# Performance work log

Measured on AMD Instinct MI355X. Metric: run time of the kernel, lower is better.

The kernel has to match this reference:

```python
import jax, jax.numpy as jnp
import numpy as np

B, S, D, E, H = 1024, 256, 1024, 1024, 1024  # batch, state, belief, embedding, hidden
T1 = 32            # clip_length => number of scan steps
POSE_TILES = 4
MIN_STD = 0.1


def _gru(x, h, wih, whh, bih, bhh):
    # torch.nn.GRUCell semantics
    gi = x @ wih.T + bih
    gh = h @ whh.T + bhh
    i_r, i_z, i_n = jnp.split(gi, 3, axis=-1)
    h_r, h_z, h_n = jnp.split(gh, 3, axis=-1)
    r = jax.nn.sigmoid(i_r + h_r)
    z = jax.nn.sigmoid(i_z + h_z)
    n = jnp.tanh(i_n + r * h_n)
    return (1.0 - z) * n + z * h


def setup_inputs() -> dict:
    key = jax.random.key(0)
    ks = iter(jax.random.split(key, 40))
    g = lambda shape, s=1.0: jax.random.normal(next(ks), shape, dtype=jnp.float32) * s
    W = 0.02
    inp = {
        'prev_state': g((B, S)),
        'prev_belief': g((B, D)),
        'observations': g((T1, B, E)),
        'poses': g((T1, B, 6)),
        'noise_post': g((T1, B, S)),
        'noise_prior': g((T1, B, S)),
        # fc_embed_state_posterior: (2S+E) -> D
        'W_esq': g((D, 2 * S + E), W), 'b_esq': jnp.zeros((D,), jnp.float32),
        # fc_embed_state_prior: (2S+6*pose_tiles) -> D
        'W_esp': g((D, 2 * S + 6 * POSE_TILES), W), 'b_esp': jnp.zeros((D,), jnp.float32),
        # GRUCell posterior / prior
        'gq_wih': g((3 * D, D), W), 'gq_whh': g((3 * D, D), W),
        'gq_bih': jnp.zeros((3 * D,), jnp.float32), 'gq_bhh': jnp.zeros((3 * D,), jnp.float32),
        'gp_wih': g((3 * D, D), W), 'gp_whh': g((3 * D, D), W),
        'gp_bih': jnp.zeros((3 * D,), jnp.float32), 'gp_bhh': jnp.zeros((3 * D,), jnp.float32),
        # belief -> hidden -> 2*state heads
        'W_ebq': g((H, D), W), 'b_ebq': jnp.zeros((H,), jnp.float32),
        'W_sq': g((2 * S, H), W), 'b_sq': jnp.zeros((2 * S,), jnp.float32),
        'W_ebp': g((H, D), W), 'b_ebp': jnp.zeros((H,), jnp.float32),
        'W_sp': g((2 * S, H), W), 'b_sp': jnp.zeros((2 * S,), jnp.float32),
    }
    return inp


def reference(prev_state, prev_belief, observations, poses, noise_post, noise_prior,
              W_esq, b_esq, W_esp, b_esp,
              gq_wih, gq_whh, gq_bih, gq_bhh,
              gp_wih, gp_whh, gp_bih, gp_bhh,
              W_ebq, b_ebq, W_sq, b_sq, W_ebp, b_ebp, W_sp, b_sp):
    relu = jax.nn.relu

    def step(carry, xs):
        s_q, s_p, b_q, b_p = carry
        obs, pose, nq, npn = xs
        # posterior branch
        h = relu(jnp.concatenate([obs, s_q, s_p], axis=1) @ W_esq.T + b_esq)
        b_q_new = _gru(h, b_q, gq_wih, gq_whh, gq_bih, gq_bhh)
        hq = relu(b_q_new @ W_ebq.T + b_ebq)
        mq, raw_sq = jnp.split(hq @ W_sq.T + b_sq, 2, axis=1)
        std_q = jax.nn.softplus(raw_sq) + MIN_STD
        s_q_new = mq + std_q * nq
        # prior branch (uses old s_q, s_p per original code)
        pose_t = jnp.tile(pose, (1, POSE_TILES))
        h2 = relu(jnp.concatenate([pose_t, s_q, s_p], axis=1) @ W_esp.T + b_esp)
        b_p_new = _gru(h2, b_p, gp_wih, gp_whh, gp_bih, gp_bhh)
        hp = relu(b_p_new @ W_ebp.T + b_ebp)
        mp, raw_sp = jnp.split(hp @ W_sp.T + b_sp, 2, axis=1)
        std_p = jax.nn.softplus(raw_sp) + MIN_STD
        s_p_new = mp + std_p * npn
        new_carry = (s_q_new, s_p_new, b_q_new, b_p_new)
        ys = (b_q_new, s_p_new, mp, std_p, s_q_new, mq, std_q)
        return new_carry, ys

    carry0 = (prev_state, prev_state, prev_belief, prev_belief)
    _, ys = jax.lax.scan(step, carry0, (observations, poses, noise_post, noise_prior))
    post_beliefs, prior_states, prior_means, prior_stds, post_states, post_means, post_stds = ys
    # order matches torch: [posterior_beliefs, prior_states, prior_means, prior_std_devs,
    #                       posterior_states, posterior_means, posterior_std_devs]
    return (post_beliefs, prior_states, prior_means, prior_stds,
            post_states, post_means, post_stds)
```

## Files before the change

### kernel.cpp

```cpp
#include <hip/hip_runtime.h>
#include <stdint.h>
#include <math.h>

typedef unsigned short ushort_t;
typedef __attribute__((ext_vector_type(8))) short bf16x8;
typedef __attribute__((ext_vector_type(4))) float f32x4;

#define T1_ 32

__device__ __forceinline__ float bf2f(ushort_t u) {
  union { unsigned int i; float f; } v; v.i = ((unsigned int)u) << 16; return v.f;
}
__device__ __forceinline__ ushort_t f2bf(float f) {
  union { float f; unsigned int i; } v; v.f = f;
  unsigned int x = v.i;
  return (ushort_t)((x + 0x7FFFu + ((x >> 16) & 1u)) >> 16);
}
__device__ __forceinline__ float sigm(float x) { return 1.f / (1.f + expf(-x)); }

__device__ __forceinline__ void gld16(const ushort_t* g, ushort_t* l) {
  __builtin_amdgcn_global_load_lds(
      (const __attribute__((address_space(1))) unsigned int*)g,
      (__attribute__((address_space(3))) unsigned int*)l, 16, 0, 0);
}

__global__ __launch_bounds__(256) void cvt_k(const float* src, ushort_t* dst,
                                             long long n, int cols, int src_ld, int src_off) {
  const long long idx = (long long)blockIdx.x * 256 + threadIdx.x;
  if (idx >= n) return;
  const long long row = idx / cols;
  const int col = (int)(idx - row * cols);
  dst[idx] = f2bf(src[row * src_ld + src_off + col]);
}

__global__ __launch_bounds__(256) void wpe_k(const float* Wesp, float* wpe) {
  const int i = blockIdx.x * 256 + threadIdx.x;
  if (i >= 1024 * 6) return;
  const int n = i / 6, j = i % 6;
  float s = 0.f;
#pragma unroll
  for (int r = 0; r < 4; ++r) s += Wesp[(long long)n * 536 + j + 6 * r];
  wpe[i] = s;
}

__global__ void marker_k(float* out, float K) {
  if (threadIdx.x == 0 && blockIdx.x == 0) out[0] = K;
}

struct MMSide {
  const ushort_t* a0; const ushort_t* a1; const ushort_t* a2;
  int kd0, kd1, kd2;
  int coff0, coff1, coff2;
  int nparts;
  const ushort_t* W; int ldw;
  const float* bias;
  ushort_t* outb;
  int dopose;
};
struct MM2Args { MMSide s[2]; const float* poses_t; const float* wpe; };

__global__ __launch_bounds__(256) void mm2_k(MM2Args g) {
  const MMSide S = g.s[blockIdx.z];
  __shared__ __align__(16) ushort_t As[2048];
  __shared__ __align__(16) ushort_t Ws[4096];
  const int tid = threadIdx.x;
  const int lane = tid & 63, wave = tid >> 6;
  const int wm = wave >> 1, wn = wave & 1;
  const int bn0 = blockIdx.x * 128, bm0 = blockIdx.y * 64;

  f32x4 acc[2][4];
#pragma unroll
  for (int i = 0; i < 2; ++i)
#pragma unroll
    for (int j = 0; j < 4; ++j) acc[i][j] = (f32x4){0.f, 0.f, 0.f, 0.f};

  const ushort_t* ap[3] = { S.a0, S.a1, S.a2 };
  const int kd[3] = { S.kd0, S.kd1, S.kd2 };
  const int cf[3] = { S.coff0, S.coff1, S.coff2 };

  const int rowA = tid >> 2, kcA = (tid & 3) * 8;
  ushort_t* ldsA  = &As[wave * 512];
  ushort_t* ldsW0 = &Ws[wave * 512];
  ushort_t* ldsW1 = &Ws[2048 + wave * 512];

#pragma unroll 1
  for (int p = 0; p < S.nparts; ++p) {
    const int kdim = kd[p];
    const ushort_t* Ap = ap[p] + (long long)bm0 * kdim + (long long)rowA * kdim + kcA;
    const ushort_t* Wp0 = S.W + cf[p] + (long long)(bn0 + rowA) * S.ldw + kcA;
    const ushort_t* Wp1 = Wp0 + (long long)64 * S.ldw;
    const int nkt = kdim >> 5;
#pragma unroll 1
    for (int kt = 0; kt < nkt; ++kt) {
      const int k0 = kt * 32;
      __syncthreads();
      gld16(Ap + k0, ldsA);
      gld16(Wp0 + k0, ldsW0);
      gld16(Wp1 + k0, ldsW1);
      __syncthreads();
      const int r15 = lane & 15, kh = (lane >> 4) * 8;
      bf16x8 a[2], b[4];
#pragma unroll
      for (int i = 0; i < 2; ++i)
        a[i] = *(const bf16x8*)&As[(wm * 32 + i * 16 + r15) * 32 + kh];
#pragma unroll
      for (int j = 0; j < 4; ++j)
        b[j] = *(const bf16x8*)&Ws[(wn * 64 + j * 16 + r15) * 32 + kh];
#pragma unroll
      for (int i = 0; i < 2; ++i)
#pragma unroll
        for (int j = 0; j < 4; ++j)
          acc[i][j] = __builtin_amdgcn_mfma_f32_16x16x32_bf16(a[i], b[j], acc[i][j], 0, 0, 0);
    }
  }

  const int r15 = lane & 15, rq = (lane >> 4) * 4;
#pragma unroll
  for (int i = 0; i < 2; ++i) {
#pragma unroll
    for (int j = 0; j < 4; ++j) {
      const int col = bn0 + wn * 64 + j * 16 + r15;
      const float bs = S.bias[col];
#pragma unroll
      for (int q = 0; q < 4; ++q) {
        const int row = bm0 + wm * 32 + i * 16 + rq + q;
        float v = acc[i][j][q] + bs;
        if (S.dopose) {
          float s = 0.f;
#pragma unroll
          for (int jj = 0; jj < 6; ++jj)
            s += g.poses_t[(long long)row * 6 + jj] * g.wpe[col * 6 + jj];
          v += s;
        }
        v = fmaxf(v, 0.f);
        S.outb[(size_t)row * 1024 + col] = f2bf(v);
      }
    }
  }
}

struct GruSide {
  const ushort_t* x;
  const ushort_t* hb;
  const float* hf;
  const ushort_t* wih; const ushort_t* whh;
  const float* bih; const float* bhh;
  float* dst; ushort_t* dstb;
};
struct Gru2Args { GruSide s[2]; };

__global__ __launch_bounds__(256) void gru2_k(Gru2Args g) {
  const GruSide S = g.s[blockIdx.z];
  __shared__ __align__(16) ushort_t Xs[2048];
  __shared__ __align__(16) ushort_t Hs[2048];
  __shared__ __align__(16) ushort_t Wt[6][2048];
  const int tid = threadIdx.x;
  const int lane = tid & 63, wave = tid >> 6;
  const int wm = wave >> 1, wn = wave & 1;
  const int bn0 = blockIdx.x * 64, bm0 = blockIdx.y * 64;

  f32x4 acc[6][2][2];
#pragma unroll
  for (int gg = 0; gg < 6; ++gg)
#pragma unroll
    for (int i = 0; i < 2; ++i)
#pragma unroll
      for (int j = 0; j < 2; ++j) acc[gg][i][j] = (f32x4){0.f, 0.f, 0.f, 0.f};

  const int rowA = tid >> 2, kc = (tid & 3) * 8;
  const long long xoff = (long long)(bm0 + rowA) * 1024 + kc;

#pragma unroll 1
  for (int kt = 0; kt < 32; ++kt) {
    const int k0 = kt * 32;
    __syncthreads();
    gld16(S.x + xoff + k0, &Xs[wave * 512]);
    gld16(S.hb + xoff + k0, &Hs[wave * 512]);
#pragma unroll
    for (int gg = 0; gg < 6; ++gg) {
      const ushort_t* base = (gg < 3) ? S.wih : S.whh;
      const int grow = (gg % 3) * 1024 + bn0 + rowA;
      gld16(base + (long long)grow * 1024 + k0 + kc, &Wt[gg][wave * 512]);
    }
    __syncthreads();
    const int r15 = lane & 15, kh = (lane >> 4) * 8;
    bf16x8 ax[2], ah[2];
#pragma unroll
    for (int i = 0; i < 2; ++i) {
      ax[i] = *(const bf16x8*)&Xs[(wm * 32 + i * 16 + r15) * 32 + kh];
      ah[i] = *(const bf16x8*)&Hs[(wm * 32 + i * 16 + r15) * 32 + kh];
    }
#pragma unroll
    for (int gg = 0; gg < 6; ++gg) {
      bf16x8 bw[2];
#pragma unroll
      for (int j = 0; j < 2; ++j)
        bw[j] = *(const bf16x8*)&Wt[gg][(wn * 32 + j * 16 + r15) * 32 + kh];
#pragma unroll
      for (int i = 0; i < 2; ++i)
#pragma unroll
        for (int j = 0; j < 2; ++j)
          acc[gg][i][j] = __builtin_amdgcn_mfma_f32_16x16x32_bf16(
              (gg < 3) ? ax[i] : ah[i], bw[j], acc[gg][i][j], 0, 0, 0);
    }
  }

  const int r15 = lane & 15, rq = (lane >> 4) * 4;
#pragma unroll
  for (int j = 0; j < 2; ++j) {
    const int col = bn0 + wn * 32 + j * 16 + r15;
    const float br  = S.bih[col],        bhr = S.bhh[col];
    const float bz  = S.bih[col + 1024], bhz = S.bhh[col + 1024];
    const float bn_ = S.bih[col + 2048], bhn = S.bhh[col + 2048];
#pragma unroll
    for (int i = 0; i < 2; ++i) {
#pragma unroll
      for (int q = 0; q < 4; ++q) {
        const int row = bm0 + wm * 32 + i * 16 + rq + q;
        const float ir = acc[0][i][j][q] + br,   hr = acc[3][i][j][q] + bhr;
        const float iz = acc[1][i][j][q] + bz,   hz = acc[4][i][j][q] + bhz;
        const float in_ = acc[2][i][j][q] + bn_, hn = acc[5][i][j][q] + bhn;
        const float r = sigm(ir + hr);
        const float z = sigm(iz + hz);
        const float ng = tanhf(in_ + r * hn);
        const long long o = (long long)row * 1024 + col;
        const float bnew = (1.f - z) * ng + z * S.hf[o];
        S.dst[o] = bnew;
        S.dstb[o] = f2bf(bnew);
      }
    }
  }
}

struct HeadSide {
  const ushort_t* hh;
  const ushort_t* Ws;
  const float* bs;
  const float* noise;
  float* omean; float* ostd; float* ostate;
  ushort_t* stateb;
};
struct Head2Args { HeadSide s[2]; };

__global__ __launch_bounds__(256) void head2_k(Head2Args g) {
  const HeadSide S = g.s[blockIdx.z];
  __shared__ __align__(16) ushort_t As[2048];
  __shared__ __align__(16) ushort_t Wt[2][2048];
  const int tid = threadIdx.x;
  const int lane = tid & 63, wave = tid >> 6;
  const int wm = wave >> 1, wn = wave & 1;
  const int bn0 = blockIdx.x * 64, bm0 = blockIdx.y * 64;

  f32x4 acc[2][2][2];
#pragma unroll
  for (int gg = 0; gg < 2; ++gg)
#pragma unroll
    for (int i = 0; i < 2; ++i)
#pragma unroll
      for (int j = 0; j < 2; ++j) acc[gg][i][j] = (f32x4){0.f, 0.f, 0.f, 0.f};

  const int rowA = tid >> 2, kc = (tid & 3) * 8;
  const long long aoff = (long long)(bm0 + rowA) * 1024 + kc;

#pragma unroll 1
  for (int kt = 0; kt < 32; ++kt) {
    const int k0 = kt * 32;
    __syncthreads();
    gld16(S.hh + aoff + k0, &As[wave * 512]);
#pragma unroll
    for (int gg = 0; gg < 2; ++gg)
      gld16(S.Ws + (long long)(gg * 256 + bn0 + rowA) * 1024 + k0 + kc, &Wt[gg][wave * 512]);
    __syncthreads();
    const int r15 = lane & 15, kh = (lane >> 4) * 8;
    bf16x8 a[2];
#pragma unroll
    for (int i = 0; i < 2; ++i)
      a[i] = *(const bf16x8*)&As[(wm * 32 + i * 16 + r15) * 32 + kh];
#pragma unroll
    for (int gg = 0; gg < 2; ++gg) {
      bf16x8 bw[2];
#pragma unroll
      for (int j = 0; j < 2; ++j)
        bw[j] = *(const bf16x8*)&Wt[gg][(wn * 32 + j * 16 + r15) * 32 + kh];
#pragma unroll
      for (int i = 0; i < 2; ++i)
#pragma unroll
        for (int j = 0; j < 2; ++j)
          acc[gg][i][j] = __builtin_amdgcn_mfma_f32_16x16x32_bf16(a[i], bw[j], acc[gg][i][j], 0, 0, 0);
    }
  }

  const int r15 = lane & 15, rq = (lane >> 4) * 4;
#pragma unroll
  for (int j = 0; j < 2; ++j) {
    const int col = bn0 + wn * 32 + j * 16 + r15;
    const float bm = S.bs[col];
    const float bsd = S.bs[col + 256];
#pragma unroll
    for (int i = 0; i < 2; ++i) {
#pragma unroll
      for (int q = 0; q < 4; ++q) {
        const int row = bm0 + wm * 32 + i * 16 + rq + q;
        const float mean = acc[0][i][j][q] + bm;
        const float rs = acc[1][i][j][q] + bsd;
        const float sp = fmaxf(rs, 0.f) + log1pf(expf(-fabsf(rs)));
        const float sd = sp + 0.1f;
        const long long o = (long long)row * 256 + col;
        const float st = mean + sd * S.noise[o];
        S.omean[o] = mean; S.ostd[o] = sd; S.ostate[o] = st;
        S.stateb[o] = f2bf(st);
      }
    }
  }
}

extern "C" void kernel_launch(void* const* d_in, const int* in_sizes, int n_in,
                              void* d_out, int out_size, void* d_ws, size_t ws_size,
                              hipStream_t stream) {
  float* out = (float*)d_out;

  int gid = 0;
  if (n_in != 26) gid = 1;
  else if (out_size != 83886080) gid = 2;
  else if (in_sizes[0] != 262144 || in_sizes[1] != 1048576 || in_sizes[2] != 33554432 ||
           in_sizes[3] != 196608 || in_sizes[4] != 8388608 || in_sizes[5] != 8388608) gid = 3;
  else if (in_sizes[6] != 1572864 || in_sizes[8] != 548864) gid = 4;
  else if (in_sizes[10] != 3145728 || in_sizes[11] != 3145728 ||
           in_sizes[14] != 3145728 || in_sizes[15] != 3145728) gid = 5;
  else if (in_sizes[18] != 1048576 || in_sizes[20] != 524288 ||
           in_sizes[22] != 1048576 || in_sizes[24] != 524288) gid = 6;
  else if (ws_size < (128ull << 20)) gid = 7;
  if (gid != 0) {
    unsigned wsMB = (unsigned)(ws_size >> 20); if (wsMB > 4095u) wsMB = 4095u;
    const float K = (float)gid * 16777216.0f + (float)wsMB;
    hipLaunchKernelGGL(marker_k, dim3(1), dim3(64), 0, stream, out, K);
    return;
  }

  const float* prev_state  = (const float*)d_in[0];
  const float* prev_belief = (const float*)d_in[1];
  const float* observations= (const float*)d_in[2];
  const float* poses       = (const float*)d_in[3];
  const float* noise_post  = (const float*)d_in[4];
  const float* noise_prior = (const float*)d_in[5];
  const float* W_esq = (const float*)d_in[6];  const float* b_esq = (const float*)d_in[7];
  const float* W_esp = (const float*)d_in[8];  const float* b_esp = (const float*)d_in[9];
  const float* gq_wih = (const float*)d_in[10]; const float* gq_whh = (const float*)d_in[11];
  const float* gq_bih = (const float*)d_in[12]; const float* gq_bhh = (const float*)d_in[13];
  const float* gp_wih = (const float*)d_in[14]; const float* gp_whh = (const float*)d_in[15];
  const float* gp_bih = (const float*)d_in[16]; const float* gp_bhh = (const float*)d_in[17];
  const float* W_ebq = (const float*)d_in[18]; const float* b_ebq = (const float*)d_in[19];
  const float* W_sq  = (const float*)d_in[20]; const float* b_sq  = (const float*)d_in[21];
  const float* W_ebp = (const float*)d_in[22]; const float* b_ebp = (const float*)d_in[23];
  const float* W_sp  = (const float*)d_in[24]; const float* b_sp  = (const float*)d_in[25];

  float* out_belief = out;
  float* out_pstate = out + 33554432LL;
  float* out_pmean  = out + 41943040LL;
  float* out_pstd   = out + 50331648LL;
  float* out_qstate = out + 58720256LL;
  float* out_qmean  = out + 67108864LL;
  float* out_qstd   = out + 75497472LL;

  char* w = (char*)d_ws;
  ushort_t* obsb  = (ushort_t*)(w);
  ushort_t* wWesq = (ushort_t*)(w + (64ull << 20));
  ushort_t* wWesp = (ushort_t*)(w + (67ull << 20));
  ushort_t* wGqih = (ushort_t*)(w + (68ull << 20));
  ushort_t* wGqhh = (ushort_t*)(w + (74ull << 20));
  ushort_t* wGpih = (ushort_t*)(w + (80ull << 20));
  ushort_t* wGphh = (ushort_t*)(w + (86ull << 20));
  ushort_t* wEbq  = (ushort_t*)(w + (92ull << 20));
  ushort_t* wEbp  = (ushort_t*)(w + (94ull << 20));
  ushort_t* wSq   = (ushort_t*)(w + (96ull << 20));
  ushort_t* wSp   = (ushort_t*)(w + (97ull << 20));
  float*    wpe   = (float*)(w + (98ull << 20));
  ushort_t* h_q   = (ushort_t*)(w + (99ull << 20));
  ushort_t* h_p   = (ushort_t*)(w + (101ull << 20));
  ushort_t* bqb[2] = { (ushort_t*)(w + (103ull << 20)), (ushort_t*)(w + (105ull << 20)) };
  ushort_t* bpb[2] = { (ushort_t*)(w + (107ull << 20)), (ushort_t*)(w + (109ull << 20)) };
  ushort_t* sqb   = (ushort_t*)(w + (111ull << 20));
  ushort_t* spb   = (ushort_t*)(w + (111ull << 20) + 524288);
  float*    bpf[2] = { (float*)(w + (112ull << 20)), (float*)(w + (116ull << 20)) };

  const dim3 blk(256);
  auto cvt = [&](const float* s, ushort_t* d, long long n, int c, int ld, int off) {
    hipLaunchKernelGGL(cvt_k, dim3((unsigned)((n + 255) / 256)), blk, 0, stream, s, d, n, c, ld, off);
  };
  cvt(observations, obsb, 33554432LL, 1024, 1024, 0);
  cvt(W_esq, wWesq, 1572864LL, 1536, 1536, 0);
  cvt(W_esp, wWesp, 524288LL, 512, 536, 24);
  cvt(gq_wih, wGqih, 3145728LL, 1024, 1024, 0);
  cvt(gq_whh, wGqhh, 3145728LL, 1024, 1024, 0);
  cvt(gp_wih, wGpih, 3145728LL, 1024, 1024, 0);
  cvt(gp_whh, wGphh, 3145728LL, 1024, 1024, 0);
  cvt(W_ebq, wEbq, 1048576LL, 1024, 1024, 0);
  cvt(W_ebp, wEbp, 1048576LL, 1024, 1024, 0);
  cvt(W_sq, wSq, 524288LL, 1024, 1024, 0);
  cvt(W_sp, wSp, 524288LL, 1024, 1024, 0);
  cvt(prev_state, sqb, 262144LL, 256, 256, 0);
  cvt(prev_state, spb, 262144LL, 256, 256, 0);
  cvt(prev_belief, bqb[1], 1048576LL, 1024, 1024, 0);
  cvt(prev_belief, bpb[1], 1048576LL, 1024, 1024, 0);
  hipLaunchKernelGGL(wpe_k, dim3(24), blk, 0, stream, W_esp, wpe);

  for (int t = 0; t < T1_; ++t) {
    const int cur = t & 1, prv = cur ^ 1;
    const ushort_t* obs_t = obsb + (long long)t * 1048576;
    const float* bq_prev_f = (t == 0) ? prev_belief : out_belief + (long long)(t - 1) * 1048576;
    const float* bp_prev_f = (t == 0) ? prev_belief : bpf[prv];

    MM2Args a{};
    a.s[0] = MMSide{ obs_t, sqb, spb, 1024, 256, 256, 0, 1024, 1280, 3,
                     wWesq, 1536, b_esq, h_q, 0 };
    a.s[1] = MMSide{ sqb, spb, nullptr, 256, 256, 0, 0, 256, 0, 2,
                     wWesp, 512, b_esp, h_p, 1 };
    a.poses_t = poses + (long long)t * 6144; a.wpe = wpe;
    hipLaunchKernelGGL(mm2_k, dim3(8, 16, 2), blk, 0, stream, a);

    Gru2Args gr{};
    gr.s[0] = GruSide{ h_q, bqb[prv], bq_prev_f, wGqih, wGqhh, gq_bih, gq_bhh,
                       out_belief + (long long)t * 1048576, bqb[cur] };
    gr.s[1] = GruSide{ h_p, bpb[prv], bp_prev_f, wGpih, wGphh, gp_bih, gp_bhh,
                       bpf[cur], bpb[cur] };
    hipLaunchKernelGGL(gru2_k, dim3(16, 16, 2), blk, 0, stream, gr);

    a = MM2Args{};
    a.s[0] = MMSide{ bqb[cur], nullptr, nullptr, 1024, 0, 0, 0, 0, 0, 1,
                     wEbq, 1024, b_ebq, h_q, 0 };
    a.s[1] = MMSide{ bpb[cur], nullptr, nullptr, 1024, 0, 0, 0, 0, 0, 1,
                     wEbp, 1024, b_ebp, h_p, 0 };
    hipLaunchKernelGGL(mm2_k, dim3(8, 16, 2), blk, 0, stream, a);

    Head2Args hd{};
    hd.s[0] = HeadSide{ h_q, wSq, b_sq, noise_post + (long long)t * 262144,
                        out_qmean + (long long)t * 262144,
                        out_qstd + (long long)t * 262144,
                        out_qstate + (long long)t * 262144, sqb };
    hd.s[1] = HeadSide{ h_p, wSp, b_sp, noise_prior + (long long)t * 262144,
                        out_pmean + (long long)t * 262144,
                        out_pstd + (long long)t * 262144,
                        out_pstate + (long long)t * 262144, spb };
    hipLaunchKernelGGL(head2_k, dim3(4, 16, 2), blk, 0, stream, hd);
  }
}
```

Baseline: 4.067 ms.

## Fuse whole recurrent scan into one persistent cooperative kernel with grid syncs

Replaces roughly 144 separate kernel launches (conversions plus four kernels per step) with a single cooperative kernel of 256 blocks of 512 threads. It runs the weight and observation conversion, then all 32 steps, separated by grid-wide barriers. It also double-buffers the LDS tiles so the next K-slice loads while MFMAs run on the current one, and retiles the GEMMs across the fixed grid. This removes launch overhead and inter-kernel gaps, but a 256-block grid may leave the GRU and embed GEMMs with fewer waves in flight than before, and grid.sync adds its own cost.

After: 7.827 ms. 1.92x slower.

```diff
diff --git a/kernel.cpp b/kernel.cpp
--- a/kernel.cpp
+++ b/kernel.cpp
@@ -1,16 +1,14 @@
 #include <hip/hip_runtime.h>
+#include <hip/hip_cooperative_groups.h>
 #include <stdint.h>
 #include <math.h>
+
+namespace cg = cooperative_groups;
 
 typedef unsigned short ushort_t;
 typedef __attribute__((ext_vector_type(8))) short bf16x8;
 typedef __attribute__((ext_vector_type(4))) float f32x4;
 
-#define T1_ 32
-
-__device__ __forceinline__ float bf2f(ushort_t u) {
-  union { unsigned int i; float f; } v; v.i = ((unsigned int)u) << 16; return v.f;
-}
 __device__ __forceinline__ ushort_t f2bf(float f) {
   union { float f; unsigned int i; } v; v.f = f;
   unsigned int x = v.i;
@@ -18,299 +16,349 @@
 }
 __device__ __forceinline__ float sigm(float x) { return 1.f / (1.f + expf(-x)); }
 
+__device__ __forceinline__ bf16x8 cvt8(const float* f) {
+  const f32x4 lo = *(const f32x4*)f;
+  const f32x4 hi = *(const f32x4*)(f + 4);
+  bf16x8 r;
+  r[0] = (short)f2bf(lo[0]); r[1] = (short)f2bf(lo[1]);
+  r[2] = (short)f2bf(lo[2]); r[3] = (short)f2bf(lo[3]);
+  r[4] = (short)f2bf(hi[0]); r[5] = (short)f2bf(hi[1]);
+  r[6] = (short)f2bf(hi[2]); r[7] = (short)f2bf(hi[3]);
+  return r;
+}
+
 __device__ __forceinline__ void gld16(const ushort_t* g, ushort_t* l) {
   __builtin_amdgcn_global_load_lds(
       (const __attribute__((address_space(1))) unsigned int*)g,
       (__attribute__((address_space(3))) unsigned int*)l, 16, 0, 0);
 }
 
-__global__ __launch_bounds__(256) void cvt_k(const float* src, ushort_t* dst,
-                                             long long n, int cols, int src_ld, int src_off) {
-  const long long idx = (long long)blockIdx.x * 256 + threadIdx.x;
-  if (idx >= n) return;
-  const long long row = idx / cols;
-  const int col = (int)(idx - row * cols);
-  dst[idx] = f2bf(src[row * src_ld + src_off + col]);
-}
-
-__global__ __launch_bounds__(256) void wpe_k(const float* Wesp, float* wpe) {
-  const int i = blockIdx.x * 256 + threadIdx.x;
-  if (i >= 1024 * 6) return;
-  const int n = i / 6, j = i % 6;
-  float s = 0.f;
-#pragma unroll
-  for (int r = 0; r < 4; ++r) s += Wesp[(long long)n * 536 + j + 6 * r];
-  wpe[i] = s;
-}
-
 __global__ void marker_k(float* out, float K) {
   if (threadIdx.x == 0 && blockIdx.x == 0) out[0] = K;
 }
 
-struct MMSide {
-  const ushort_t* a0; const ushort_t* a1; const ushort_t* a2;
-  int kd0, kd1, kd2;
-  int coff0, coff1, coff2;
-  int nparts;
-  const ushort_t* W; int ldw;
-  const float* bias;
-  ushort_t* outb;
-  int dopose;
+struct MegaArgs {
+  const float *prev_state, *prev_belief, *obs, *poses, *noise_q, *noise_p;
+  const float *W_esq, *b_esq, *W_esp, *b_esp;
+  const float *gq_bih, *gq_bhh, *gp_bih, *gp_bhh;
+  const float *gq_wih, *gq_whh, *gp_wih, *gp_whh;
+  const float *W_ebq, *b_ebq, *W_sq, *b_sq, *W_ebp, *b_ebp, *W_sp, *b_sp;
+  float* out;
+  ushort_t *obsb, *wWesq, *wWesp, *wGqih, *wGqhh, *wGpih, *wGphh, *wEbq, *wEbp, *wSq, *wSp;
+  float* wpe;
+  ushort_t *h_q, *h_p, *bqb0, *bqb1, *bpb0, *bpb1, *sqb, *spb;
+  float *bpf0, *bpf1;
 };
-struct MM2Args { MMSide s[2]; const float* poses_t; const float* wpe; };
-
-__global__ __launch_bounds__(256) void mm2_k(MM2Args g) {
-  const MMSide S = g.s[blockIdx.z];
-  __shared__ __align__(16) ushort_t As[2048];
-  __shared__ __align__(16) ushort_t Ws[4096];
-  const int tid = threadIdx.x;
-  const int lane = tid & 63, wave = tid >> 6;
-  const int wm = wave >> 1, wn = wave & 1;
-  const int bn0 = blockIdx.x * 128, bm0 = blockIdx.y * 64;
-
-  f32x4 acc[2][4];
-#pragma unroll
-  for (int i = 0; i < 2; ++i)
-#pragma unroll
-    for (int j = 0; j < 4; ++j) acc[i][j] = (f32x4){0.f, 0.f, 0.f, 0.f};
-
-  const ushort_t* ap[3] = { S.a0, S.a1, S.a2 };
-  const int kd[3] = { S.kd0, S.kd1, S.kd2 };
-  const int cf[3] = { S.coff0, S.coff1, S.coff2 };
-
-  const int rowA = tid >> 2, kcA = (tid & 3) * 8;
-  ushort_t* ldsA  = &As[wave * 512];
-  ushort_t* ldsW0 = &Ws[wave * 512];
-  ushort_t* ldsW1 = &Ws[2048 + wave * 512];
-
-#pragma unroll 1
-  for (int p = 0; p < S.nparts; ++p) {
-    const int kdim = kd[p];
-    const ushort_t* Ap = ap[p] + (long long)bm0 * kdim + (long long)rowA * kdim + kcA;
-    const ushort_t* Wp0 = S.W + cf[p] + (long long)(bn0 + rowA) * S.ldw + kcA;
-    const ushort_t* Wp1 = Wp0 + (long long)64 * S.ldw;
-    const int nkt = kdim >> 5;
-#pragma unroll 1
-    for (int kt = 0; kt < nkt; ++kt) {
-      const int k0 = kt * 32;
-      __syncthreads();
-      gld16(Ap + k0, ldsA);
-      gld16(Wp0 + k0, ldsW0);
-      gld16(Wp1 + k0, ldsW1);
-      __syncthreads();
-      const int r15 = lane & 15, kh = (lane >> 4) * 8;
-      bf16x8 a[2], b[4];
-#pragma unroll
-      for (int i = 0; i < 2; ++i)
-        a[i] = *(const bf16x8*)&As[(wm * 32 + i * 16 + r15) * 32 + kh];
-#pragma unroll
-      for (int j = 0; j < 4; ++j)
-        b[j] = *(const bf16x8*)&Ws[(wn * 64 + j * 16 + r15) * 32 + kh];
-#pragma unroll
-      for (int i = 0; i < 2; ++i)
-#pragma unroll
-        for (int j = 0; j < 4; ++j)
-          acc[i][j] = __builtin_amdgcn_mfma_f32_16x16x32_bf16(a[i], b[j], acc[i][j], 0, 0, 0);
+
+__global__ __launch_bounds__(512) void mega_k(MegaArgs A) {
+  __shared__ __align__(16) ushort_t lds[2][20480];
+  cg::grid_group grid = cg::this_grid();
+  const int bid = blockIdx.x, tid = threadIdx.x;
+  const int lane = tid & 63, wv = tid >> 6;
+  const int r15 = lane & 15, kh = (lane >> 4) * 8, rq = (lane >> 4) * 4;
+  const int l2 = lane >> 2, l3 = (lane & 3) * 8;
+  const int gtid = bid * 512 + tid;
+
+  {
+    auto cv = [&](const float* s, ushort_t* d, int n8, int c8, int ld, int off) {
+      for (int c = gtid; c < n8; c += 131072) {
+        const int row = c / c8, col = (c - row * c8) * 8;
+        *(bf16x8*)(d + (size_t)row * (c8 * 8) + col) = cvt8(s + (size_t)row * ld + off + col);
+      }
+    };
+    cv(A.obs, A.obsb, 4194304, 128, 1024, 0);
+    cv(A.W_esq, A.wWesq, 196608, 192, 1536, 0);
+    cv(A.W_esp, A.wWesp, 65536, 64, 536, 24);
+    cv(A.gq_wih, A.wGqih, 393216, 128, 1024, 0);
+    cv(A.gq_whh, A.wGqhh, 393216, 128, 1024, 0);
+    cv(A.gp_wih, A.wGpih, 393216, 128, 1024, 0);
+    cv(A.gp_whh, A.wGphh, 393216, 128, 1024, 0);
+    cv(A.W_ebq, A.wEbq, 131072, 128, 1024, 0);
+    cv(A.W_ebp, A.wEbp, 131072, 128, 1024, 0);
+    cv(A.W_sq, A.wSq, 65536, 128, 1024, 0);
+    cv(A.W_sp, A.wSp, 65536, 128, 1024, 0);
+    cv(A.prev_state, A.sqb, 32768, 32, 256, 0);
+    cv(A.prev_state, A.spb, 32768, 32, 256, 0);
+    cv(A.prev_belief, A.bqb1, 131072, 128, 1024, 0);
+    cv(A.prev_belief, A.bpb1, 131072, 128, 1024, 0);
+    for (int i = gtid; i < 6144; i += 131072) {
+      const int n = i / 6, j = i - n * 6;
+      float s = 0.f;
+#pragma unroll
+      for (int r = 0; r < 4; ++r) s += A.W_esp[(size_t)n * 536 + j + 6 * r];
+      A.wpe[i] = s;
     }
   }
-
-  const int r15 = lane & 15, rq = (lane >> 4) * 4;
-#pragma unroll
-  for (int i = 0; i < 2; ++i) {
-#pragma unroll
-    for (int j = 0; j < 4; ++j) {
-      const int col = bn0 + wn * 64 + j * 16 + r15;
-      const float bs = S.bias[col];
-#pragma unroll
-      for (int q = 0; q < 4; ++q) {
-        const int row = bm0 + wm * 32 + i * 16 + rq + q;
-        float v = acc[i][j][q] + bs;
-        if (S.dopose) {
-          float s = 0.f;
-#pragma unroll
-          for (int jj = 0; jj < 6; ++jj)
-            s += g.poses_t[(long long)row * 6 + jj] * g.wpe[col * 6 + jj];
-          v += s;
-        }
-        v = fmaxf(v, 0.f);
-        S.outb[(size_t)row * 1024 + col] = f2bf(v);
+  grid.sync();
+
+  ushort_t* bqb[2] = { A.bqb0, A.bqb1 };
+  ushort_t* bpb[2] = { A.bpb0, A.bpb1 };
+  float* bpf[2] = { A.bpf0, A.bpf1 };
+
+  for (int t = 0; t < 32; ++t) {
+    const int cur = t & 1, prv = cur ^ 1;
+
+    auto embed_like = [&](const ushort_t* A0, const ushort_t* A1, const ushort_t* A2,
+                          int kd0, int c1, int c2, int nkt, int cf0, int cf1, int cf2,
+                          const ushort_t* W, int ldw, const float* bias, ushort_t* outp,
+                          int dopose, const float* poses_t) {
+      const int loc = bid & 127;
+      const int bn0 = (loc & 7) * 128, bm0 = (loc >> 3) * 64;
+      const int wm = wv >> 2, wn = wv & 3;
+
+      auto stage = [&](int buf, int ktg) {
+        const ushort_t* ab; int kd, cf, ktl;
+        if (ktg < c1) { ab = A0; kd = kd0; cf = cf0; ktl = ktg; }
+        else if (ktg < c2) { ab = A1; kd = 256; cf = cf1; ktl = ktg - c1; }
+        else { ab = A2; kd = 256; cf = cf2; ktl = ktg - c2; }
+        const int k0 = ktl * 32;
+        if (wv < 4)
+          gld16(ab + (size_t)(bm0 + wv * 16 + l2) * kd + k0 + l3, &lds[buf][wv * 512]);
+        else
+          gld16(W + cf + (size_t)(bn0 + (wv - 4) * 16 + l2) * ldw + k0 + l3,
+                &lds[buf][2048 + (wv - 4) * 512]);
+        if (wv < 4)
+          gld16(W + cf + (size_t)(bn0 + (wv + 4) * 16 + l2) * ldw + k0 + l3,
+                &lds[buf][2048 + (wv + 4) * 512]);
+      };
+
+      f32x4 acc[2][2];
+#pragma unroll
+      for (int i = 0; i < 2; ++i)
+#pragma unroll
+        for (int j = 0; j < 2; ++j) acc[i][j] = (f32x4){0.f, 0.f, 0.f, 0.f};
+
+      stage(0, 0); __syncthreads();
+      int cb = 0;
+#pragma unroll 1
+      for (int ktg = 0; ktg < nkt; ++ktg) {
+        if (ktg + 1 < nkt) stage(cb ^ 1, ktg + 1);
+        bf16x8 a[2], b[2];
+#pragma unroll
+        for (int i = 0; i < 2; ++i)
+          a[i] = *(const bf16x8*)&lds[cb][(wm * 32 + i * 16 + r15) * 32 + kh];
+#pragma unroll
+        for (int j = 0; j < 2; ++j)
+          b[j] = *(const bf16x8*)&lds[cb][2048 + (wn * 32 + j * 16 + r15) * 32 + kh];
+#pragma unroll
+        for (int i = 0; i < 2; ++i)
+#pragma unroll
+          for (int j = 0; j < 2; ++j)
+            acc[i][j] = __builtin_amdgcn_mfma_f32_16x16x32_bf16(a[i], b[j], acc[i][j], 0, 0, 0);
+        __syncthreads(); cb ^= 1;
+      }
+
+#pragma unroll
+      for (int i = 0; i < 2; ++i) {
+#pragma unroll
+        for (int j = 0; j < 2; ++j) {
+          const int col = bn0 + wn * 32 + j * 16 + r15;
+          const float bs = bias[col];
+#pragma unroll
+          for (int q = 0; q < 4; ++q) {
+            const int row = bm0 + wm * 32 + i * 16 + rq + q;
+            float v = acc[i][j][q] + bs;
+            if (dopose) {
+              float s = 0.f;
+#pragma unroll
+              for (int jj = 0; jj < 6; ++jj)
+                s += poses_t[(size_t)row * 6 + jj] * A.wpe[col * 6 + jj];
+              v += s;
+            }
+            v = fmaxf(v, 0.f);
+            outp[(size_t)row * 1024 + col] = f2bf(v);
+          }
+        }
+      }
+    };
+
+    if ((bid >> 7) == 0)
+      embed_like(A.obsb + (size_t)t * 1048576, A.sqb, A.spb,
+                 1024, 32, 40, 48, 0, 1024, 1280,
+                 A.wWesq, 1536, A.b_esq, A.h_q, 0, nullptr);
+    else
+      embed_like(A.sqb, A.spb, A.spb,
+                 256, 8, 16, 16, 0, 256, 256,
+                 A.wWesp, 512, A.b_esp, A.h_p, 1, A.poses + (size_t)t * 6144);
+    grid.sync();
+
+    {
+      const int side = bid & 1;
+      const int bn0 = ((bid >> 1) & 15) * 64;
+      const int bm0 = (bid >> 5) * 128;
+      const ushort_t *x, *hb, *wih, *whh;
+      const float *hf, *bih, *bhh;
+      float* dst; ushort_t* dstb;
+      if (side == 0) {
+        x = A.h_q; hb = bqb[prv];
+        hf = t ? (A.out + (size_t)(t - 1) * 1048576) : A.prev_belief;
+        wih = A.wGqih; whh = A.wGqhh; bih = A.gq_bih; bhh = A.gq_bhh;
+        dst = A.out + (size_t)t * 1048576; dstb = bqb[cur];
+      } else {
+        x = A.h_p; hb = bpb[prv];
+        hf = t ? bpf[prv] : A.prev_belief;
+        wih = A.wGpih; whh = A.wGphh; bih = A.gp_bih; bhh = A.gp_bhh;
+        dst = bpf[cur]; dstb = bpb[cur];
+      }
+      const int wm = wv >> 1, wn = wv & 1;
+
+      auto stage = [&](int buf, int kt) {
+        const int k0 = kt * 32;
+#pragma unroll
+        for (int u = 0; u < 5; ++u) {
+          const int c = wv * 5 + u;
+          if (c < 8)
+            gld16(x + (size_t)(bm0 + c * 16 + l2) * 1024 + k0 + l3, &lds[buf][c * 512]);
+          else if (c < 16)
+            gld16(hb + (size_t)(bm0 + (c - 8) * 16 + l2) * 1024 + k0 + l3, &lds[buf][c * 512]);
+          else {
+            const int wch = c - 16, gg = wch >> 2, rc = wch & 3;
+            const ushort_t* base = (gg < 3) ? wih : whh;
+            const int gr = (gg < 3 ? gg : gg - 3) * 1024 + bn0 + rc * 16 + l2;
+            gld16(base + (size_t)gr * 1024 + k0 + l3, &lds[buf][8192 + gg * 2048 + rc * 512]);
+          }
+        }
+      };
+
+      f32x4 aR[2][2], aZ[2][2], aNI[2][2], aNH[2][2];
+#pragma unroll
+      for (int i = 0; i < 2; ++i)
+#pragma unroll
+        for (int j = 0; j < 2; ++j) {
+          aR[i][j] = (f32x4){0.f,0.f,0.f,0.f}; aZ[i][j] = (f32x4){0.f,0.f,0.f,0.f};
+          aNI[i][j] = (f32x4){0.f,0.f,0.f,0.f}; aNH[i][j] = (f32x4){0.f,0.f,0.f,0.f};
+        }
+
+      stage(0, 0); __syncthreads();
+      int cb = 0;
+#pragma unroll 1
+      for (int kt = 0; kt < 32; ++kt) {
+        if (kt + 1 < 32) stage(cb ^ 1, kt + 1);
+        bf16x8 ax[2], ah[2], w[6][2];
+#pragma unroll
+        for (int i = 0; i < 2; ++i) {
+          ax[i] = *(const bf16x8*)&lds[cb][(wm * 32 + i * 16 + r15) * 32 + kh];
+          ah[i] = *(const bf16x8*)&lds[cb][4096 + (wm * 32 + i * 16 + r15) * 32 + kh];
+        }
+#pragma unroll
+        for (int g = 0; g < 6; ++g)
+#pragma unroll
+          for (int j = 0; j < 2; ++j)
+            w[g][j] = *(const bf16x8*)&lds[cb][8192 + g * 2048 + (wn * 32 + j * 16 + r15) * 32 + kh];
+#pragma unroll
+        for (int i = 0; i < 2; ++i)
+#pragma unroll
+          for (int j = 0; j < 2; ++j) {
+            aR[i][j]  = __builtin_amdgcn_mfma_f32_16x16x32_bf16(ax[i], w[0][j], aR[i][j], 0, 0, 0);
+            aR[i][j]  = __builtin_amdgcn_mfma_f32_16x16x32_bf16(ah[i], w[3][j], aR[i][j], 0, 0, 0);
+            aZ[i][j]  = __builtin_amdgcn_mfma_f32_16x16x32_bf16(ax[i], w[1][j], aZ[i][j], 0, 0, 0);
+            aZ[i][j]  = __builtin_amdgcn_mfma_f32_16x16x32_bf16(ah[i], w[4][j], aZ[i][j], 0, 0, 0);
+            aNI[i][j] = __builtin_amdgcn_mfma_f32_16x16x32_bf16(ax[i], w[2][j], aNI[i][j], 0, 0, 0);
+            aNH[i][j] = __builtin_amdgcn_mfma_f32_16x16x32_bf16(ah[i], w[5][j], aNH[i][j], 0, 0, 0);
+          }
+        __syncthreads(); cb ^= 1;
+      }
+
+#pragma unroll
+      for (int j = 0; j < 2; ++j) {
+        const int col = bn0 + wn * 32 + j * 16 + r15;
+        const float brz = bih[col] + bhh[col];
+        const float bzz = bih[col + 1024] + bhh[col + 1024];
+        const float bni = bih[col + 2048], bnh = bhh[col + 2048];
+#pragma unroll
+        for (int i = 0; i < 2; ++i) {
+#pragma unroll
+          for (int q = 0; q < 4; ++q) {
+            const int row = bm0 + wm * 32 + i * 16 + rq + q;
+            const float r = sigm(aR[i][j][q] + brz);
+            const float z = sigm(aZ[i][j][q] + bzz);
+            const float ng = tanhf(aNI[i][j][q] + bni + r * (aNH[i][j][q] + bnh));
+            const size_t o = (size_t)row * 1024 + col;
+            const float bnew = (1.f - z) * ng + z * hf[o];
+            dst[o] = bnew;
+            dstb[o] = f2bf(bnew);
+          }
+        }
       }
     }
-  }
-}
-
-struct GruSide {
-  const ushort_t* x;
-  const ushort_t* hb;
-  const float* hf;
-  const ushort_t* wih; const ushort_t* whh;
-  const float* bih; const float* bhh;
-  float* dst; ushort_t* dstb;
-};
-struct Gru2Args { GruSide s[2]; };
-
-__global__ __launch_bounds__(256) void gru2_k(Gru2Args g) {
-  const GruSide S = g.s[blockIdx.z];
-  __shared__ __align__(16) ushort_t Xs[2048];
-  __shared__ __align__(16) ushort_t Hs[2048];
-  __shared__ __align__(16) ushort_t Wt[6][2048];
-  const int tid = threadIdx.x;
-  const int lane = tid & 63, wave = tid >> 6;
-  const int wm = wave >> 1, wn = wave & 1;
-  const int bn0 = blockIdx.x * 64, bm0 = blockIdx.y * 64;
-
-  f32x4 acc[6][2][2];
-#pragma unroll
-  for (int gg = 0; gg < 6; ++gg)
-#pragma unroll
-    for (int i = 0; i < 2; ++i)
-#pragma unroll
-      for (int j = 0; j < 2; ++j) acc[gg][i][j] = (f32x4){0.f, 0.f, 0.f, 0.f};
-
-  const int rowA = tid >> 2, kc = (tid & 3) * 8;
-  const long long xoff = (long long)(bm0 + rowA) * 1024 + kc;
-
+    grid.sync();
+
+    if ((bid >> 7) == 0)
+      embed_like(bqb[cur], bqb[cur], bqb[cur], 1024, 32, 32, 32, 0, 0, 0,
+                 A.wEbq, 1024, A.b_ebq, A.h_q, 0, nullptr);
+    else
+      embed_like(bpb[cur], bpb[cur], bpb[cur], 1024, 32, 32, 32, 0, 0, 0,
+                 A.wEbp, 1024, A.b_ebp, A.h_p, 0, nullptr);
+    grid.sync();
+
+    if (bid < 128) {
+      const int side = bid & 1;
+      const int t64 = bid >> 1;
+      const int bn0 = (t64 & 3) * 64, bm0 = (t64 >> 2) * 64;
+      const ushort_t* hh = side ? A.h_p : A.h_q;
+      const ushort_t* Ws = side ? A.wSp : A.wSq;
+      const float* bs = side ? A.b_sp : A.b_sq;
+      const float* noise = (side ? A.noise_p : A.noise_q) + (size_t)t * 262144;
+      float* omean  = A.out + (side ? 41943040LL : 67108864LL) + (size_t)t * 262144;
+      float* ostd   = A.out + (side ? 50331648LL : 75497472LL) + (size_t)t * 262144;
+      float* ostate = A.out + (side ? 33554432LL : 58720256LL) + (size_t)t * 262144;
+      ushort_t* stb = side ? A.spb : A.sqb;
+      const int wm = wv >> 2, wn = wv & 3;
+
+      auto stage = [&](int buf, int kt) {
+        const int k0 = kt * 32;
+        if (wv < 4)
+          gld16(hh + (size_t)(bm0 + wv * 16 + l2) * 1024 + k0 + l3, &lds[buf][wv * 512]);
+        else
+          gld16(Ws + (size_t)(bn0 + (wv - 4) * 16 + l2) * 1024 + k0 + l3,
+                &lds[buf][2048 + (wv - 4) * 512]);
+        if (wv < 4)
+          gld16(Ws + (size_t)(256 + bn0 + wv * 16 + l2) * 1024 + k0 + l3,
+                &lds[buf][4096 + wv * 512]);
+      };
+
+      f32x4 aM[2], aS[2];
+#pragma unroll
+      for (int i = 0; i < 2; ++i) { aM[i] = (f32x4){0.f,0.f,0.f,0.f}; aS[i] = (f32x4){0.f,0.f,0.f,0.f}; }
+
+      stage(0, 0); __syncthreads();
+      int cb = 0;
 #pragma unroll 1
-  for (int kt = 0; kt < 32; ++kt) {
-    const int k0 = kt * 32;
-    __syncthreads();
-    gld16(S.x + xoff + k0, &Xs[wave * 512]);
-    gld16(S.hb + xoff + k0, &Hs[wave * 512]);
-#pragma unroll
-    for (int gg = 0; gg < 6; ++gg) {
-      const ushort_t* base = (gg < 3) ? S.wih : S.whh;
-      const int grow = (gg % 3) * 1024 + bn0 + rowA;
-      gld16(base + (long long)grow * 1024 + k0 + kc, &Wt[gg][wave * 512]);
+      for (int kt = 0; kt < 32; ++kt) {
+        if (kt + 1 < 32) stage(cb ^ 1, kt + 1);
+        bf16x8 a[2];
+#pragma unroll
+        for (int i = 0; i < 2; ++i)
+          a[i] = *(const bf16x8*)&lds[cb][(wm * 32 + i * 16 + r15) * 32 + kh];
+        const bf16x8 bm8 = *(const bf16x8*)&lds[cb][2048 + (wn * 16 + r15) * 32 + kh];
+        const bf16x8 br8 = *(const bf16x8*)&lds[cb][4096 + (wn * 16 + r15) * 32 + kh];
+#pragma unroll
+        for (int i = 0; i < 2; ++i) {
+          aM[i] = __builtin_amdgcn_mfma_f32_16x16x32_bf16(a[i], bm8, aM[i], 0, 0, 0);
+          aS[i] = __builtin_amdgcn_mfma_f32_16x16x32_bf16(a[i], br8, aS[i], 0, 0, 0);
+        }
+        __syncthreads(); cb ^= 1;
+      }
+
+      const int col = bn0 + wn * 16 + r15;
+      const float bm_ = bs[col], bsd = bs[col + 256];
+#pragma unroll
+      for (int i = 0; i < 2; ++i) {
+#pragma unroll
+        for (int q = 0; q < 4; ++q) {
+          const int row = bm0 + wm * 32 + i * 16 + rq + q;
+          const float mean = aM[i][q] + bm_;
+          const float rs = aS[i][q] + bsd;
+          const float sp = fmaxf(rs, 0.f) + log1pf(expf(-fabsf(rs)));
+          const float sd = sp + 0.1f;
+          const size_t o = (size_t)row * 256 + col;
+          const float st = mean + sd * noise[o];
+          omean[o] = mean; ostd[o] = sd; ostate[o] = st;
+          stb[o] = f2bf(st);
+        }
+      }
     }
-    __syncthreads();
-    const int r15 = lane & 15, kh = (lane >> 4) * 8;
-    bf16x8 ax[2], ah[2];
-#pragma unroll
-    for (int i = 0; i < 2; ++i) {
-      ax[i] = *(const bf16x8*)&Xs[(wm * 32 + i * 16 + r15) * 32 + kh];
-      ah[i] = *(const bf16x8*)&Hs[(wm * 32 + i * 16 + r15) * 32 + kh];
-    }
-#pragma unroll
-    for (int gg = 0; gg < 6; ++gg) {
-      bf16x8 bw[2];
-#pragma unroll
-      for (int j = 0; j < 2; ++j)
-        bw[j] = *(const bf16x8*)&Wt[gg][(wn * 32 + j * 16 + r15) * 32 + kh];
-#pragma unroll
-      for (int i = 0; i < 2; ++i)
-#pragma unroll
-        for (int j = 0; j < 2; ++j)
-          acc[gg][i][j] = __builtin_amdgcn_mfma_f32_16x16x32_bf16(
-              (gg < 3) ? ax[i] : ah[i], bw[j], acc[gg][i][j], 0, 0, 0);
-    }
-  }
-
-  const int r15 = lane & 15, rq = (lane >> 4) * 4;
-#pragma unroll
-  for (int j = 0; j < 2; ++j) {
-    const int col = bn0 + wn * 32 + j * 16 + r15;
-    const float br  = S.bih[col],        bhr = S.bhh[col];
-    const float bz  = S.bih[col + 1024], bhz = S.bhh[col + 1024];
-    const float bn_ = S.bih[col + 2048], bhn = S.bhh[col + 2048];
-#pragma unroll
-    for (int i = 0; i < 2; ++i) {
-#pragma unroll
-      for (int q = 0; q < 4; ++q) {
-        const int row = bm0 + wm * 32 + i * 16 + rq + q;
-        const float ir = acc[0][i][j][q] + br,   hr = acc[3][i][j][q] + bhr;
-        const float iz = acc[1][i][j][q] + bz,   hz = acc[4][i][j][q] + bhz;
-        const float in_ = acc[2][i][j][q] + bn_, hn = acc[5][i][j][q] + bhn;
-        const float r = sigm(ir + hr);
-        const float z = sigm(iz + hz);
-        const float ng = tanhf(in_ + r * hn);
-        const long long o = (long long)row * 1024 + col;
-        const float bnew = (1.f - z) * ng + z * S.hf[o];
-        S.dst[o] = bnew;
-        S.dstb[o] = f2bf(bnew);
-      }
-    }
-  }
-}
-
-struct HeadSide {
-  const ushort_t* hh;
-  const ushort_t* Ws;
-  const float* bs;
-  const float* noise;
-  float* omean; float* ostd; float* ostate;
-  ushort_t* stateb;
-};
-struct Head2Args { HeadSide s[2]; };
-
-__global__ __launch_bounds__(256) void head2_k(Head2Args g) {
-  const HeadSide S = g.s[blockIdx.z];
-  __shared__ __align__(16) ushort_t As[2048];
-  __shared__ __align__(16) ushort_t Wt[2][2048];
-  const int tid = threadIdx.x;
-  const int lane = tid & 63, wave = tid >> 6;
-  const int wm = wave >> 1, wn = wave & 1;
-  const int bn0 = blockIdx.x * 64, bm0 = blockIdx.y * 64;
-
-  f32x4 acc[2][2][2];
-#pragma unroll
-  for (int gg = 0; gg < 2; ++gg)
-#pragma unroll
-    for (int i = 0; i < 2; ++i)
-#pragma unroll
-      for (int j = 0; j < 2; ++j) acc[gg][i][j] = (f32x4){0.f, 0.f, 0.f, 0.f};
-
-  const int rowA = tid >> 2, kc = (tid & 3) * 8;
-  const long long aoff = (long long)(bm0 + rowA) * 1024 + kc;
-
-#pragma unroll 1
-  for (int kt = 0; kt < 32; ++kt) {
-    const int k0 = kt * 32;
-    __syncthreads();
-    gld16(S.hh + aoff + k0, &As[wave * 512]);
-#pragma unroll
-    for (int gg = 0; gg < 2; ++gg)
-      gld16(S.Ws + (long long)(gg * 256 + bn0 + rowA) * 1024 + k0 + kc, &Wt[gg][wave * 512]);
-    __syncthreads();
-    const int r15 = lane & 15, kh = (lane >> 4) * 8;
-    bf16x8 a[2];
-#pragma unroll
-    for (int i = 0; i < 2; ++i)
-      a[i] = *(const bf16x8*)&As[(wm * 32 + i * 16 + r15) * 32 + kh];
-#pragma unroll
-    for (int gg = 0; gg < 2; ++gg) {
-      bf16x8 bw[2];
-#pragma unroll
-      for (int j = 0; j < 2; ++j)
-        bw[j] = *(const bf16x8*)&Wt[gg][(wn * 32 + j * 16 + r15) * 32 + kh];
-#pragma unroll
-      for (int i = 0; i < 2; ++i)
-#pragma unroll
-        for (int j = 0; j < 2; ++j)
-          acc[gg][i][j] = __builtin_amdgcn_mfma_f32_16x16x32_bf16(a[i], bw[j], acc[gg][i][j], 0, 0, 0);
-    }
-  }
-
-  const int r15 = lane & 15, rq = (lane >> 4) * 4;
-#pragma unroll
-  for (int j = 0; j < 2; ++j) {
-    const int col = bn0 + wn * 32 + j * 16 + r15;
-    const float bm = S.bs[col];
-    const float bsd = S.bs[col + 256];
-#pragma unroll
-    for (int i = 0; i < 2; ++i) {
-#pragma unroll
-      for (int q = 0; q < 4; ++q) {
-        const int row = bm0 + wm * 32 + i * 16 + rq + q;
-        const float mean = acc[0][i][j][q] + bm;
-        const float rs = acc[1][i][j][q] + bsd;
-        const float sp = fmaxf(rs, 0.f) + log1pf(expf(-fabsf(rs)));
-        const float sd = sp + 0.1f;
-        const long long o = (long long)row * 256 + col;
-        const float st = mean + sd * S.noise[o];
-        S.omean[o] = mean; S.ostd[o] = sd; S.ostate[o] = st;
-        S.stateb[o] = f2bf(st);
-      }
-    }
+    grid.sync();
   }
 }
 
@@ -337,110 +385,48 @@
     return;
   }
 
-  const float* prev_state  = (const float*)d_in[0];
-  const float* prev_belief = (const float*)d_in[1];
-  const float* observations= (const float*)d_in[2];
-  const float* poses       = (const float*)d_in[3];
-  const float* noise_post  = (const float*)d_in[4];
-  const float* noise_prior = (const float*)d_in[5];
-  const float* W_esq = (const float*)d_in[6];  const float* b_esq = (const float*)d_in[7];
-  const float* W_esp = (const float*)d_in[8];  const float* b_esp = (const float*)d_in[9];
-  const float* gq_wih = (const float*)d_in[10]; const float* gq_whh = (const float*)d_in[11];
-  const float* gq_bih = (const float*)d_in[12]; const float* gq_bhh = (const float*)d_in[13];
-  const float* gp_wih = (const float*)d_in[14]; const float* gp_whh = (const float*)d_in[15];
-  const float* gp_bih = (const float*)d_in[16]; const float* gp_bhh = (const float*)d_in[17];
-  const float* W_ebq = (const float*)d_in[18]; const float* b_ebq = (const float*)d_in[19];
-  const float* W_sq  = (const float*)d_in[20]; const float* b_sq  = (const float*)d_in[21];
-  const float* W_ebp = (const float*)d_in[22]; const float* b_ebp = (const float*)d_in[23];
-  const float* W_sp  = (const float*)d_in[24]; const float* b_sp  = (const float*)d_in[25];
-
-  float* out_belief = out;
-  float* out_pstate = out + 33554432LL;
-  float* out_pmean  = out + 41943040LL;
-  float* out_pstd   = out + 50331648LL;
-  float* out_qstate = out + 58720256LL;
-  float* out_qmean  = out + 67108864LL;
-  float* out_qstd   = out + 75497472LL;
-
   char* w = (char*)d_ws;
-  ushort_t* obsb  = (ushort_t*)(w);
-  ushort_t* wWesq = (ushort_t*)(w + (64ull << 20));
-  ushort_t* wWesp = (ushort_t*)(w + (67ull << 20));
-  ushort_t* wGqih = (ushort_t*)(w + (68ull << 20));
-  ushort_t* wGqhh = (ushort_t*)(w + (74ull << 20));
-  ushort_t* wGpih = (ushort_t*)(w + (80ull << 20));
-  ushort_t* wGphh = (ushort_t*)(w + (86ull << 20));
-  ushort_t* wEbq  = (ushort_t*)(w + (92ull << 20));
-  ushort_t* wEbp  = (ushort_t*)(w + (94ull << 20));
-  ushort_t* wSq   = (ushort_t*)(w + (96ull << 20));
-  ushort_t* wSp   = (ushort_t*)(w + (97ull << 20));
-  float*    wpe   = (float*)(w + (98ull << 20));
-  ushort_t* h_q   = (ushort_t*)(w + (99ull << 20));
-  ushort_t* h_p   = (ushort_t*)(w + (101ull << 20));
-  ushort_t* bqb[2] = { (ushort_t*)(w + (103ull << 20)), (ushort_t*)(w + (105ull << 20)) };
-  ushort_t* bpb[2] = { (ushort_t*)(w + (107ull << 20)), (ushort_t*)(w + (109ull << 20)) };
-  ushort_t* sqb   = (ushort_t*)(w + (111ull << 20));
-  ushort_t* spb   = (ushort_t*)(w + (111ull << 20) + 524288);
-  float*    bpf[2] = { (float*)(w + (112ull << 20)), (float*)(w + (116ull << 20)) };
-
-  const dim3 blk(256);
-  auto cvt = [&](const float* s, ushort_t* d, long long n, int c, int ld, int off) {
-    hipLaunchKernelGGL(cvt_k, dim3((unsigned)((n + 255) / 256)), blk, 0, stream, s, d, n, c, ld, off);
-  };
-  cvt(observations, obsb, 33554432LL, 1024, 1024, 0);
-  cvt(W_esq, wWesq, 1572864LL, 1536, 1536, 0);
-  cvt(W_esp, wWesp, 524288LL, 512, 536, 24);
-  cvt(gq_wih, wGqih, 3145728LL, 1024, 1024, 0);
-  cvt(gq_whh, wGqhh, 3145728LL, 1024, 1024, 0);
-  cvt(gp_wih, wGpih, 3145728LL, 1024, 1024, 0);
-  cvt(gp_whh, wGphh, 3145728LL, 1024, 1024, 0);
-  cvt(W_ebq, wEbq, 1048576LL, 1024, 1024, 0);
-  cvt(W_ebp, wEbp, 1048576LL, 1024, 1024, 0);
-  cvt(W_sq, wSq, 524288LL, 1024, 1024, 0);
-  cvt(W_sp, wSp, 524288LL, 1024, 1024, 0);
-  cvt(prev_state, sqb, 262144LL, 256, 256, 0);
-  cvt(prev_state, spb, 262144LL, 256, 256, 0);
-  cvt(prev_belief, bqb[1], 1048576LL, 1024, 1024, 0);
-  cvt(prev_belief, bpb[1], 1048576LL, 1024, 1024, 0);
-  hipLaunchKernelGGL(wpe_k, dim3(24), blk, 0, stream, W_esp, wpe);
-
-  for (int t = 0; t < T1_; ++t) {
-    const int cur = t & 1, prv = cur ^ 1;
-    const ushort_t* obs_t = obsb + (long long)t * 1048576;
-    const float* bq_prev_f = (t == 0) ? prev_belief : out_belief + (long long)(t - 1) * 1048576;
-    const float* bp_prev_f = (t == 0) ? prev_belief : bpf[prv];
-
-    MM2Args a{};
-    a.s[0] = MMSide{ obs_t, sqb, spb, 1024, 256, 256, 0, 1024, 1280, 3,
-                     wWesq, 1536, b_esq, h_q, 0 };
-    a.s[1] = MMSide{ sqb, spb, nullptr, 256, 256, 0, 0, 256, 0, 2,
-                     wWesp, 512, b_esp, h_p, 1 };
-    a.poses_t = poses + (long long)t * 6144; a.wpe = wpe;
-    hipLaunchKernelGGL(mm2_k, dim3(8, 16, 2), blk, 0, stream, a);
-
-    Gru2Args gr{};
-    gr.s[0] = GruSide{ h_q, bqb[prv], bq_prev_f, wGqih, wGqhh, gq_bih, gq_bhh,
-                       out_belief + (long long)t * 1048576, bqb[cur] };
-    gr.s[1] = GruSide{ h_p, bpb[prv], bp_prev_f, wGpih, wGphh, gp_bih, gp_bhh,
-                       bpf[cur], bpb[cur] };
-    hipLaunchKernelGGL(gru2_k, dim3(16, 16, 2), blk, 0, stream, gr);
-
-    a = MM2Args{};
-    a.s[0] = MMSide{ bqb[cur], nullptr, nullptr, 1024, 0, 0, 0, 0, 0, 1,
-                     wEbq, 1024, b_ebq, h_q, 0 };
-    a.s[1] = MMSide{ bpb[cur], nullptr, nullptr, 1024, 0, 0, 0, 0, 0, 1,
-                     wEbp, 1024, b_ebp, h_p, 0 };
-    hipLaunchKernelGGL(mm2_k, dim3(8, 16, 2), blk, 0, stream, a);
-
-    Head2Args hd{};
-    hd.s[0] = HeadSide{ h_q, wSq, b_sq, noise_post + (long long)t * 262144,
-                        out_qmean + (long long)t * 262144,
-                        out_qstd + (long long)t * 262144,
-                        out_qstate + (long long)t * 262144, sqb };
-    hd.s[1] = HeadSide{ h_p, wSp, b_sp, noise_prior + (long long)t * 262144,
-                        out_pmean + (long long)t * 262144,
-                        out_pstd + (long long)t * 262144,
-                        out_pstate + (long long)t * 262144, spb };
-    hipLaunchKernelGGL(head2_k, dim3(4, 16, 2), blk, 0, stream, hd);
-  }
-}
+  MegaArgs A{};
+  A.prev_state  = (const float*)d_in[0];
+  A.prev_belief = (const float*)d_in[1];
+  A.obs         = (const float*)d_in[2];
+  A.poses       = (const float*)d_in[3];
+  A.noise_q     = (const float*)d_in[4];
+  A.noise_p     = (const float*)d_in[5];
+  A.W_esq = (const float*)d_in[6];  A.b_esq = (const float*)d_in[7];
+  A.W_esp = (const float*)d_in[8];  A.b_esp = (const float*)d_in[9];
+  A.gq_wih = (const float*)d_in[10]; A.gq_whh = (const float*)d_in[11];
+  A.gq_bih = (const float*)d_in[12]; A.gq_bhh = (const float*)d_in[13];
+  A.gp_wih = (const float*)d_in[14]; A.gp_whh = (const float*)d_in[15];
+  A.gp_bih = (const float*)d_in[16]; A.gp_bhh = (const float*)d_in[17];
+  A.W_ebq = (const float*)d_in[18]; A.b_ebq = (const float*)d_in[19];
+  A.W_sq  = (const float*)d_in[20]; A.b_sq  = (const float*)d_in[21];
+  A.W_ebp = (const float*)d_in[22]; A.b_ebp = (const float*)d_in[23];
+  A.W_sp  = (const float*)d_in[24]; A.b_sp  = (const float*)d_in[25];
+  A.out = out;
+  A.obsb  = (ushort_t*)(w);
+  A.wWesq = (ushort_t*)(w + (64ull << 20));
+  A.wWesp = (ushort_t*)(w + (67ull << 20));
+  A.wGqih = (ushort_t*)(w + (68ull << 20));
+  A.wGqhh = (ushort_t*)(w + (74ull << 20));
+  A.wGpih = (ushort_t*)(w + (80ull << 20));
+  A.wGphh = (ushort_t*)(w + (86ull << 20));
+  A.wEbq  = (ushort_t*)(w + (92ull << 20));
+  A.wEbp  = (ushort_t*)(w + (94ull << 20));
+  A.wSq   = (ushort_t*)(w + (96ull << 20));
+  A.wSp   = (ushort_t*)(w + (97ull << 20));
+  A.wpe   = (float*)(w + (98ull << 20));
+  A.h_q   = (ushort_t*)(w + (99ull << 20));
+  A.h_p   = (ushort_t*)(w + (101ull << 20));
+  A.bqb0  = (ushort_t*)(w + (103ull << 20));
+  A.bqb1  = (ushort_t*)(w + (105ull << 20));
+  A.bpb0  = (ushort_t*)(w + (107ull << 20));
+  A.bpb1  = (ushort_t*)(w + (109ull << 20));
+  A.sqb   = (ushort_t*)(w + (111ull << 20));
+  A.spb   = (ushort_t*)(w + (111ull << 20) + 524288);
+  A.bpf0  = (float*)(w + (112ull << 20));
+  A.bpf1  = (float*)(w + (116ull << 20));
+
+  void* params[] = { (void*)&A };
+  hipLaunchCooperativeKernel((const void*)mega_k, dim3(256), dim3(512), params, 0, stream);
+}
```
